# Performance work log

Measured on AMD Instinct MI355X. Metric: run time of the kernel, lower is better.

Reference implementation:

```python
import jax, jax.numpy as jnp
import numpy as np
from jax import lax

T, B, E, H, V, TAGS = 256, 64, 1024, 1024, 50000, 50


def setup_inputs() -> dict:
    key = jax.random.key(0)
    ks = jax.random.split(key, 16)
    s = 0.02
    return {
        "X": jax.random.randint(ks[0], (T, B), 0, V),
        "lengths": jnp.full((B,), T, dtype=jnp.int64 if jax.config.jax_enable_x64 else jnp.int32),
        "embedding": jax.random.normal(ks[1], (V, E), dtype=jnp.float32) * s,
        "w_ih": jax.random.normal(ks[2], (H, E), dtype=jnp.float32) * s,
        "w_hh": jax.random.normal(ks[3], (H, H), dtype=jnp.float32) * s,
        "w_ch": jax.random.normal(ks[4], (H, H), dtype=jnp.float32) * s,
        "w_c2h": jax.random.normal(ks[5], (H, H), dtype=jnp.float32) * s,
        "b_ih": jax.random.normal(ks[6], (H,), dtype=jnp.float32) * s,
        "b_hh": jax.random.normal(ks[7], (H,), dtype=jnp.float32) * s,
        "b_ch": jax.random.normal(ks[8], (H,), dtype=jnp.float32) * s,
        "b_c2h": jax.random.normal(ks[9], (H,), dtype=jnp.float32) * s,
        "dense_w": jax.random.normal(ks[10], (TAGS, H), dtype=jnp.float32) * s,
        "dense_b": jax.random.normal(ks[11], (TAGS,), dtype=jnp.float32) * s,
        "h0": jax.random.normal(ks[12], (B, H), dtype=jnp.float32),
        "c0": jax.random.normal(ks[13], (B, H), dtype=jnp.float32),
    }


def reference(X, lengths, embedding, w_ih, w_hh, w_ch, w_c2h,
              b_ih, b_hh, b_ch, b_c2h, dense_w, dense_b, h0, c0):
    # Embedding lookup: X is time-major [T, B] -> emb [T, B, E]
    emb = embedding[X]

    def step(carry, x_t):
        hx, cx = carry
        pre = x_t @ w_ih.T + b_ih + hx @ w_hh.T + b_hh          # [B, H]
        # In the source, ingate and forgetgate are identical expressions
        gate_if = jax.nn.sigmoid(pre + cx @ w_ch.T + b_ch)
        cellgate = jnp.tanh(pre)
        cy = gate_if * cx + gate_if * cellgate
        outgate = jax.nn.sigmoid(pre + cy @ w_c2h.T + b_c2h)
        hy = outgate * jnp.tanh(cy)
        return (hy, cy), hy

    _, out = lax.scan(step, (h0, c0), emb)                       # out: [T, B, H]
    flat = out.reshape(-1, out.shape[-1])                        # [T*B, H]
    # dropout_rate=0 / eval mode -> identity
    logits = flat @ dense_w.T + dense_b                          # [T*B, TAGS]
    return jax.nn.softmax(logits, axis=1)
```

## Files before the change

### kernel.cpp

```cpp
#include <hip/hip_runtime.h>
#include <hip/hip_cooperative_groups.h>

typedef __bf16 bf16;
typedef __bf16 bf16x8 __attribute__((ext_vector_type(8)));
typedef float f32x4 __attribute__((ext_vector_type(4)));
typedef unsigned int u32;
typedef unsigned long long u64;
typedef unsigned int u32x4 __attribute__((ext_vector_type(4)));

#define TT 256
#define NTAGS 50

#define OFF_WIH   0ull
#define OFF_WHH   (OFF_WIH  + 2097152ull)
#define OFF_WCH   (OFF_WHH  + 2097152ull)
#define OFF_WC2H  (OFF_WCH  + 2097152ull)
#define OFF_DW    (OFF_WC2H + 2097152ull)
#define OFF_XW    (OFF_DW   + 131072ull)
#define OFF_HISTB (OFF_XW   + 33554432ull)
#define OFF_HB    (OFF_HISTB + 33554432ull)
#define OFF_CB    (OFF_HB   + 262144ull)
#define OFF_BAR   (OFF_CB   + 262144ull)
#define N_FLAG_WORDS (4 * 64 * 32)

__device__ __forceinline__ u64 cohload(const u64* p) {
  return __hip_atomic_load(p, __ATOMIC_RELAXED, __HIP_MEMORY_SCOPE_AGENT);
}
__device__ __forceinline__ void cohstore(u64* p, u64 v) {
  __hip_atomic_store(p, v, __ATOMIC_RELAXED, __HIP_MEMORY_SCOPE_AGENT);
}
__device__ __forceinline__ bf16x8 cohload_v8(const bf16* p) {
  union { u64 q[2]; bf16x8 v; } u;
  const u64* q = (const u64*)p;
  u.q[0] = cohload(q);
  u.q[1] = cohload(q + 1);
  return u.v;
}
__device__ __forceinline__ u32x4 cohload_q4(const bf16* p) {
  union { u64 q[2]; u32x4 v; } u;
  const u64* q = (const u64*)p;
  u.q[0] = cohload(q);
  u.q[1] = cohload(q + 1);
  return u.v;
}

__global__ void k_prep(const float* __restrict__ wih, const float* __restrict__ whh,
                       const float* __restrict__ wch, const float* __restrict__ wc2h,
                       const float* __restrict__ dw, const float* __restrict__ h0,
                       const float* __restrict__ c0, char* __restrict__ ws) {
  const long N_W = 4194304, N_DW = 65536, N_S = 65536;
  const long TOT = N_W + N_DW + 2 * N_S + N_FLAG_WORDS;
  long stride = (long)gridDim.x * blockDim.x;
  for (long idx = (long)blockIdx.x * blockDim.x + threadIdx.x; idx < TOT; idx += stride) {
    if (idx < N_W) {
      long m = idx >> 20, e = idx & 1048575;
      const float* s = (m == 0) ? wih : (m == 1) ? whh : (m == 2) ? wch : wc2h;
      ((bf16*)(ws + OFF_WIH))[idx] = (bf16)s[e];
    } else if (idx < N_W + N_DW) {
      long j = idx - N_W; long r = j >> 10, e = j & 1023;
      ((bf16*)(ws + OFF_DW))[j] = (bf16)((r < NTAGS) ? dw[r * 1024 + e] : 0.f);
    } else if (idx < N_W + N_DW + N_S) {
      long j = idx - N_W - N_DW;
      ((bf16*)(ws + OFF_HB))[j] = (bf16)h0[j];
    } else if (idx < N_W + N_DW + 2 * N_S) {
      long j = idx - N_W - N_DW - N_S;
      ((bf16*)(ws + OFF_CB))[j] = (bf16)c0[j];
    } else {
      long j = idx - N_W - N_DW - 2 * N_S;
      ((u32*)(ws + OFF_BAR))[j] = 0u;
    }
  }
}

__global__ __launch_bounds__(256) void k_xw(const int* __restrict__ X,
                                            const float* __restrict__ emb,
                                            const float* __restrict__ b_ih,
                                            const float* __restrict__ b_hh,
                                            char* __restrict__ ws) {
  const bf16* wih = (const bf16*)(ws + OFF_WIH);
  bf16* xw = (bf16*)(ws + OFF_XW);
  int l = threadIdx.x & 63, wv = threadIdx.x >> 6;
  int i0 = blockIdx.x * 64 + wv * 16;
  int h0 = blockIdx.y * 64;
  const float* ap = emb + (long)X[i0 + (l & 15)] * 1024 + ((l >> 4) * 8);
  const bf16* bp = wih + (long)(h0 + (l & 15)) * 1024 + ((l >> 4) * 8);
  f32x4 zero = {0.f, 0.f, 0.f, 0.f};
  f32x4 acc[4] = {zero, zero, zero, zero};
  for (int k = 0; k < 1024; k += 32) {
    f32x4 f0 = *(const f32x4*)(ap + k);
    f32x4 f1 = *(const f32x4*)(ap + k + 4);
    bf16x8 a;
#pragma unroll
    for (int q = 0; q < 4; ++q) { a[q] = (bf16)f0[q]; a[4 + q] = (bf16)f1[q]; }
#pragma unroll
    for (int j = 0; j < 4; ++j) {
      bf16x8 b = *(const bf16x8*)(bp + j * 16 * 1024 + k);
      acc[j] = __builtin_amdgcn_mfma_f32_16x16x32_bf16(a, b, acc[j], 0, 0, 0);
    }
  }
#pragma unroll
  for (int j = 0; j < 4; ++j)
#pragma unroll
    for (int r = 0; r < 4; ++r) {
      int row = i0 + (l >> 4) * 4 + r;
      int col = h0 + j * 16 + (l & 15);
      xw[(long)row * 1024 + col] = (bf16)(acc[j][r] + b_ih[col] + b_hh[col]);
    }
}

__global__ __launch_bounds__(256, 1) void k_rnn(const float* __restrict__ b_ch,
                                                const float* __restrict__ b_c2h,
                                                const float* __restrict__ c0,
                                                char* __restrict__ ws) {
  const bf16* xw = (const bf16*)(ws + OFF_XW);
  bf16* histb = (bf16*)(ws + OFF_HISTB);
  bf16* HB = (bf16*)(ws + OFF_HB);
  bf16* CB = (bf16*)(ws + OFF_CB);
  int g = blockIdx.x & 3, j = blockIdx.x >> 2;
  u32* flags = (u32*)(ws + OFF_BAR) + g * 64 * 32;

  int l = threadIdx.x & 63, wv = threadIdx.x >> 6;
  int b0 = g * 16, h0b = j * 16;
  int e = threadIdx.x;
  int eoff = (b0 + (e >> 4)) * 1024 + h0b + (e & 15);
  int gh = h0b + (e & 15);

  __shared__ float red[4][2][256];
  __shared__ bf16 xfer[256];

  int lane_r = l & 15;
  int koff = wv * 256 + ((l >> 4) * 8);
  long arow = (long)(b0 + lane_r) * 1024 + koff;

  u32x4 whh_r[8], wch_r[8], wc2h_r[8], cfr[8];
  {
    const bf16* p1 = (const bf16*)(ws + OFF_WHH)  + (long)(h0b + lane_r) * 1024 + koff;
    const bf16* p2 = (const bf16*)(ws + OFF_WCH)  + (long)(h0b + lane_r) * 1024 + koff;
    const bf16* p3 = (const bf16*)(ws + OFF_WC2H) + (long)(h0b + lane_r) * 1024 + koff;
#pragma unroll
    for (int kk = 0; kk < 8; ++kk) {
      whh_r[kk]  = *(const u32x4*)(p1 + kk * 32);
      wch_r[kk]  = *(const u32x4*)(p2 + kk * 32);
      wc2h_r[kk] = *(const u32x4*)(p3 + kk * 32);
      cfr[kk] = cohload_q4(CB + arow + kk * 32);
    }
  }

  float bch_v = b_ch[gh], bc2h_v = b_c2h[gh];
  float c_reg = c0[eoff];
  f32x4 zero = {0.f, 0.f, 0.f, 0.f};

  for (int t = 0; t < TT; ++t) {
    asm volatile("" : "+v"(whh_r[0]), "+v"(whh_r[1]), "+v"(whh_r[2]), "+v"(whh_r[3]),
                      "+v"(whh_r[4]), "+v"(whh_r[5]), "+v"(whh_r[6]), "+v"(whh_r[7]),
                      "+v"(wch_r[0]), "+v"(wch_r[1]), "+v"(wch_r[2]), "+v"(wch_r[3]),
                      "+v"(wch_r[4]), "+v"(wch_r[5]), "+v"(wch_r[6]), "+v"(wch_r[7]));
    asm volatile("" : "+v"(wc2h_r[0]), "+v"(wc2h_r[1]), "+v"(wc2h_r[2]), "+v"(wc2h_r[3]),
                      "+v"(wc2h_r[4]), "+v"(wc2h_r[5]), "+v"(wc2h_r[6]), "+v"(wc2h_r[7]));
    asm volatile("" : "+v"(cfr[0]), "+v"(cfr[1]), "+v"(cfr[2]), "+v"(cfr[3]),
                      "+v"(cfr[4]), "+v"(cfr[5]), "+v"(cfr[6]), "+v"(cfr[7]));

    long slot1 = (long)((t + 1) & 1) * 65536;
    float xwv = (float)xw[(long)t * 65536 + eoff];
    u32 tkA = 2u * t + 1u, tkB = 2u * t + 2u;
    const bf16* hx = HB + (long)(t & 1) * 65536;

    f32x4 ap_ = zero, ac_ = zero;
#pragma unroll
    for (int kk = 0; kk < 8; ++kk) {
      bf16x8 a1 = cohload_v8(hx + arow + kk * 32);
      ap_ = __builtin_amdgcn_mfma_f32_16x16x32_bf16(
          a1, __builtin_bit_cast(bf16x8, whh_r[kk]), ap_, 0, 0, 0);
      ac_ = __builtin_amdgcn_mfma_f32_16x16x32_bf16(
          __builtin_bit_cast(bf16x8, cfr[kk]), __builtin_bit_cast(bf16x8, wch_r[kk]), ac_, 0, 0, 0);
    }
#pragma unroll
    for (int r = 0; r < 4; ++r) {
      int ei = ((l >> 4) * 4 + r) * 16 + (l & 15);
      red[wv][0][ei] = ap_[r];
      red[wv][1][ei] = ac_[r];
    }
    __syncthreads();
    float pre = red[0][0][e] + red[1][0][e] + red[2][0][e] + red[3][0][e] + xwv;
    float cgm = red[0][1][e] + red[1][1][e] + red[2][1][e] + red[3][1][e] + bch_v;
    float gif = 1.f / (1.f + expf(-(pre + cgm)));
    float cy = gif * (c_reg + tanhf(pre));
    c_reg = cy;
    xfer[e] = (bf16)cy;
    __syncthreads();
    if (e < 64)
      cohstore((u64*)(CB + slot1 + (long)(b0 + (e >> 2)) * 1024 + h0b) + (e & 3),
               ((u64*)xfer)[e]);
    asm volatile("s_waitcnt vmcnt(0)" ::: "memory");
    if (e == 0)
      __hip_atomic_store(&flags[j * 32], tkA, __ATOMIC_RELAXED, __HIP_MEMORY_SCOPE_AGENT);
    if (e < 64) {
      const u32* my = &flags[e * 32];
      while (!__all(__hip_atomic_load(my, __ATOMIC_RELAXED, __HIP_MEMORY_SCOPE_AGENT) >= tkA))
        __builtin_amdgcn_s_sleep(1);
    }
    asm volatile("" ::: "memory");
    __syncthreads();

    f32x4 ao = zero;
#pragma unroll
    for (int kk = 0; kk < 8; ++kk) {
      cfr[kk] = cohload_q4(CB + slot1 + arow + kk * 32);
      ao = __builtin_amdgcn_mfma_f32_16x16x32_bf16(
          __builtin_bit_cast(bf16x8, cfr[kk]), __builtin_bit_cast(bf16x8, wc2h_r[kk]), ao, 0, 0, 0);
    }
#pragma unroll
    for (int r = 0; r < 4; ++r)
      red[wv][0][((l >> 4) * 4 + r) * 16 + (l & 15)] = ao[r];
    __syncthreads();
    float o = red[0][0][e] + red[1][0][e] + red[2][0][e] + red[3][0][e] + bc2h_v;
    float og = 1.f / (1.f + expf(-(pre + o)));
    bf16 hb = (bf16)(og * tanhf(cy));
    xfer[e] = hb;
    __syncthreads();
    if (t < TT - 1) {
      if (e < 64)
        cohstore((u64*)(HB + slot1 + (long)(b0 + (e >> 2)) * 1024 + h0b) + (e & 3),
                 ((u64*)xfer)[e]);
      asm volatile("s_waitcnt vmcnt(0)" ::: "memory");
      if (e == 0)
        __hip_atomic_store(&flags[j * 32], tkB, __ATOMIC_RELAXED, __HIP_MEMORY_SCOPE_AGENT);
      if (e < 64) {
        const u32* my = &flags[e * 32];
        while (!__all(__hip_atomic_load(my, __ATOMIC_RELAXED, __HIP_MEMORY_SCOPE_AGENT) >= tkB))
          __builtin_amdgcn_s_sleep(1);
      }
      asm volatile("" ::: "memory");
      __syncthreads();
    }
    histb[(long)t * 65536 + eoff] = hb;
  }
}

__global__ __launch_bounds__(256) void k_out(const float* __restrict__ dense_b,
                                             const char* __restrict__ ws,
                                             float* __restrict__ out) {
  const bf16* h  = (const bf16*)(ws + OFF_HISTB);
  const bf16* dw = (const bf16*)(ws + OFF_DW);
  int l = threadIdx.x & 63, wv = threadIdx.x >> 6;
  int i0 = blockIdx.x * 64 + wv * 16;
  const bf16* ap = h  + (long)(i0 + (l & 15)) * 1024 + ((l >> 4) * 8);
  const bf16* bp = dw + (long)(l & 15) * 1024 + ((l >> 4) * 8);
  f32x4 zero = {0.f, 0.f, 0.f, 0.f};
  f32x4 acc[4] = {zero, zero, zero, zero};
  for (int k = 0; k < 1024; k += 32) {
    bf16x8 a = *(const bf16x8*)(ap + k);
#pragma unroll
    for (int j = 0; j < 4; ++j) {
      bf16x8 b = *(const bf16x8*)(bp + j * 16 * 1024 + k);
      acc[j] = __builtin_amdgcn_mfma_f32_16x16x32_bf16(a, b, acc[j], 0, 0, 0);
    }
  }
  int tag0 = l & 15;
#pragma unroll
  for (int r = 0; r < 4; ++r) {
    int row = i0 + (l >> 4) * 4 + r;
    float lg[4], ex[4];
    float mx = -1e30f;
#pragma unroll
    for (int j = 0; j < 4; ++j) {
      int tag = j * 16 + tag0;
      lg[j] = (tag < NTAGS) ? (acc[j][r] + dense_b[tag]) : -1e30f;
      mx = fmaxf(mx, lg[j]);
    }
    for (int m = 1; m < 16; m <<= 1) mx = fmaxf(mx, __shfl_xor(mx, m, 64));
    float s = 0.f;
#pragma unroll
    for (int j = 0; j < 4; ++j) {
      int tag = j * 16 + tag0;
      ex[j] = (tag < NTAGS) ? expf(lg[j] - mx) : 0.f;
      s += ex[j];
    }
    for (int m = 1; m < 16; m <<= 1) s += __shfl_xor(s, m, 64);
    float inv = 1.f / s;
#pragma unroll
    for (int j = 0; j < 4; ++j) {
      int tag = j * 16 + tag0;
      if (tag < NTAGS) out[(long)row * 50 + tag] = ex[j] * inv;
    }
  }
}

extern "C" void kernel_launch(void* const* d_in, const int* in_sizes, int n_in,
                              void* d_out, int out_size, void* d_ws, size_t ws_size,
                              hipStream_t stream) {
  const int*   X        = (const int*)d_in[0];
  const float* embedding = (const float*)d_in[2];
  const float* w_ih  = (const float*)d_in[3];
  const float* w_hh  = (const float*)d_in[4];
  const float* w_ch  = (const float*)d_in[5];
  const float* w_c2h = (const float*)d_in[6];
  const float* b_ih  = (const float*)d_in[7];
  const float* b_hh  = (const float*)d_in[8];
  const float* b_ch  = (const float*)d_in[9];
  const float* b_c2h = (const float*)d_in[10];
  const float* dense_w = (const float*)d_in[11];
  const float* dense_b = (const float*)d_in[12];
  const float* h0 = (const float*)d_in[13];
  const float* c0 = (const float*)d_in[14];
  char* ws = (char*)d_ws;
  float* out = (float*)d_out;

  k_prep<<<2048, 256, 0, stream>>>(w_ih, w_hh, w_ch, w_c2h, dense_w, h0, c0, ws);
  k_xw<<<dim3(256, 16), 256, 0, stream>>>(X, embedding, b_ih, b_hh, ws);

  void* args[] = {(void*)&b_ch, (void*)&b_c2h, (void*)&c0, (void*)&ws};
  hipLaunchCooperativeKernel((const void*)k_rnn, dim3(256), dim3(256), args, 0, stream);

  k_out<<<256, 256, 0, stream>>>(dense_b, ws, out);
}
```

Baseline: 2.292 ms.

## Hold embedding row in registers across all column tiles in k_xw; overlap history store with barrier

k_xw now launches one block per 64-row group and keeps the converted bf16 embedding rows in registers (32 bf16x8 per lane). It then loops over all 16 column tiles, so each embedding row is gathered and converted once instead of 16 times. This cuts the gather traffic but leaves only 256 blocks and raises register pressure, which may limit parallelism and latency hiding. In k_rnn, the per-step history store is moved before the flag spin-wait so its latency overlaps the barrier. The offset macros are rewritten as literal constants with the same values.

```diff
diff --git a/kernel.cpp b/kernel.cpp
--- a/kernel.cpp
+++ b/kernel.cpp
@@ -12,15 +12,15 @@
 #define NTAGS 50
 
 #define OFF_WIH   0ull
-#define OFF_WHH   (OFF_WIH  + 2097152ull)
-#define OFF_WCH   (OFF_WHH  + 2097152ull)
-#define OFF_WC2H  (OFF_WCH  + 2097152ull)
-#define OFF_DW    (OFF_WC2H + 2097152ull)
-#define OFF_XW    (OFF_DW   + 131072ull)
-#define OFF_HISTB (OFF_XW   + 33554432ull)
-#define OFF_HB    (OFF_HISTB + 33554432ull)
-#define OFF_CB    (OFF_HB   + 262144ull)
-#define OFF_BAR   (OFF_CB   + 262144ull)
+#define OFF_WHH   2097152ull
+#define OFF_WCH   4194304ull
+#define OFF_WC2H  6291456ull
+#define OFF_DW    8388608ull
+#define OFF_XW    8519680ull
+#define OFF_HISTB 42074112ull
+#define OFF_HB    75628544ull
+#define OFF_CB    75890688ull
+#define OFF_BAR   76152832ull
 #define N_FLAG_WORDS (4 * 64 * 32)
 
 __device__ __forceinline__ u64 cohload(const u64* p) {
@@ -72,40 +72,49 @@
   }
 }
 
-__global__ __launch_bounds__(256) void k_xw(const int* __restrict__ X,
-                                            const float* __restrict__ emb,
-                                            const float* __restrict__ b_ih,
-                                            const float* __restrict__ b_hh,
-                                            char* __restrict__ ws) {
+__global__ __launch_bounds__(256, 1) void k_xw(const int* __restrict__ X,
+                                               const float* __restrict__ emb,
+                                               const float* __restrict__ b_ih,
+                                               const float* __restrict__ b_hh,
+                                               char* __restrict__ ws) {
   const bf16* wih = (const bf16*)(ws + OFF_WIH);
   bf16* xw = (bf16*)(ws + OFF_XW);
   int l = threadIdx.x & 63, wv = threadIdx.x >> 6;
   int i0 = blockIdx.x * 64 + wv * 16;
-  int h0 = blockIdx.y * 64;
   const float* ap = emb + (long)X[i0 + (l & 15)] * 1024 + ((l >> 4) * 8);
-  const bf16* bp = wih + (long)(h0 + (l & 15)) * 1024 + ((l >> 4) * 8);
+
+  bf16x8 a_reg[32];
+#pragma unroll
+  for (int k = 0; k < 32; ++k) {
+    f32x4 f0 = *(const f32x4*)(ap + k * 32);
+    f32x4 f1 = *(const f32x4*)(ap + k * 32 + 4);
+    bf16x8 a;
+#pragma unroll
+    for (int q = 0; q < 4; ++q) { a[q] = (bf16)f0[q]; a[4 + q] = (bf16)f1[q]; }
+    a_reg[k] = a;
+  }
+
   f32x4 zero = {0.f, 0.f, 0.f, 0.f};
-  f32x4 acc[4] = {zero, zero, zero, zero};
-  for (int k = 0; k < 1024; k += 32) {
-    f32x4 f0 = *(const f32x4*)(ap + k);
-    f32x4 f1 = *(const f32x4*)(ap + k + 4);
-    bf16x8 a;
-#pragma unroll
-    for (int q = 0; q < 4; ++q) { a[q] = (bf16)f0[q]; a[4 + q] = (bf16)f1[q]; }
-#pragma unroll
-    for (int j = 0; j < 4; ++j) {
-      bf16x8 b = *(const bf16x8*)(bp + j * 16 * 1024 + k);
-      acc[j] = __builtin_amdgcn_mfma_f32_16x16x32_bf16(a, b, acc[j], 0, 0, 0);
-    }
-  }
-#pragma unroll
-  for (int j = 0; j < 4; ++j)
-#pragma unroll
-    for (int r = 0; r < 4; ++r) {
-      int row = i0 + (l >> 4) * 4 + r;
-      int col = h0 + j * 16 + (l & 15);
-      xw[(long)row * 1024 + col] = (bf16)(acc[j][r] + b_ih[col] + b_hh[col]);
-    }
+  for (int ct = 0; ct < 16; ++ct) {
+    int h0 = ct * 64;
+    const bf16* bp = wih + (long)(h0 + (l & 15)) * 1024 + ((l >> 4) * 8);
+    f32x4 acc[4] = {zero, zero, zero, zero};
+#pragma unroll
+    for (int k = 0; k < 32; ++k)
+#pragma unroll
+      for (int j = 0; j < 4; ++j) {
+        bf16x8 b = *(const bf16x8*)(bp + j * 16 * 1024 + k * 32);
+        acc[j] = __builtin_amdgcn_mfma_f32_16x16x32_bf16(a_reg[k], b, acc[j], 0, 0, 0);
+      }
+#pragma unroll
+    for (int j = 0; j < 4; ++j)
+#pragma unroll
+      for (int r = 0; r < 4; ++r) {
+        int row = i0 + (l >> 4) * 4 + r;
+        int col = h0 + j * 16 + (l & 15);
+        xw[(long)row * 1024 + col] = (bf16)(acc[j][r] + b_ih[col] + b_hh[col]);
+      }
+  }
 }
 
 __global__ __launch_bounds__(256, 1) void k_rnn(const float* __restrict__ b_ch,
@@ -225,6 +234,7 @@
       asm volatile("s_waitcnt vmcnt(0)" ::: "memory");
       if (e == 0)
         __hip_atomic_store(&flags[j * 32], tkB, __ATOMIC_RELAXED, __HIP_MEMORY_SCOPE_AGENT);
+      histb[(long)t * 65536 + eoff] = hb;
       if (e < 64) {
         const u32* my = &flags[e * 32];
         while (!__all(__hip_atomic_load(my, __ATOMIC_RELAXED, __HIP_MEMORY_SCOPE_AGENT) >= tkB))
@@ -232,8 +242,9 @@
       }
       asm volatile("" ::: "memory");
       __syncthreads();
-    }
-    histb[(long)t * 65536 + eoff] = hb;
+    } else {
+      histb[(long)t * 65536 + eoff] = hb;
+    }
   }
 }
 
@@ -307,7 +318,7 @@
   float* out = (float*)d_out;
 
   k_prep<<<2048, 256, 0, stream>>>(w_ih, w_hh, w_ch, w_c2h, dense_w, h0, c0, ws);
-  k_xw<<<dim3(256, 16), 256, 0, stream>>>(X, embedding, b_ih, b_hh, ws);
+  k_xw<<<256, 256, 0, stream>>>(X, embedding, b_ih, b_hh, ws);
 
   void* args[] = {(void*)&b_ch, (void*)&b_c2h, (void*)&c0, (void*)&ws};
   hipLaunchCooperativeKernel((const void*)k_rnn, dim3(256), dim3(256), args, 0, stream);
```

Result: no change. 2.285 ms, median of 2 (-0.3%).
